# Optimization experiments

Hardware: AMD Instinct MI355X
Metric: run time of the kernel (lower is better)

The kernel has to match this reference:

```python
import jax, jax.numpy as jnp
import numpy as np

N_NODES = 50000
N_EDGES = 800000
N_GRAPHS = 512
D_IN = 128
D_HID = 128
D_OUT = 128
N_CLS = 2


def _deg_inv_sqrt(idx, n):
    deg = jax.ops.segment_sum(jnp.ones(idx.shape[0], jnp.float32), idx, num_segments=n)
    return jnp.where(deg > 0, jax.lax.rsqrt(jnp.maximum(deg, 1.0)), 0.0)


def gcn_conv(x, src, dst, W, b, out_norm, in_norm):
    # DGL GraphConv, norm='both': D_out^{-1/2} on src, sum-aggregate, D_in^{-1/2} on dst, then XW + b
    h = x * out_norm[:, None]                                   # [N, d]
    agg = jax.ops.segment_sum(h[src], dst, num_segments=x.shape[0])  # SpMM: gather + scatter-add
    agg = agg * in_norm[:, None]
    return agg @ W + b


def setup_inputs() -> dict:
    key = jax.random.key(0)
    ks = jax.random.split(key, 8)
    features = jax.random.normal(ks[0], (N_NODES, D_IN), jnp.float32)
    src = jax.random.randint(ks[1], (N_EDGES,), 0, N_NODES, jnp.int32)
    dst = jax.random.randint(ks[2], (N_EDGES,), 0, N_NODES, jnp.int32)
    graph_ids = jnp.sort(jax.random.randint(ks[3], (N_NODES,), 0, N_GRAPHS, jnp.int32))
    W1 = jax.random.normal(ks[4], (D_IN, D_HID), jnp.float32) / np.sqrt(D_IN)
    W2 = jax.random.normal(ks[5], (D_HID, D_OUT), jnp.float32) / np.sqrt(D_HID)
    Wc = jax.random.normal(ks[6], (D_OUT, N_CLS), jnp.float32) / np.sqrt(D_OUT)
    return {
        'features': features, 'src': src, 'dst': dst, 'graph_ids': graph_ids,
        'W1': W1, 'b1': jnp.zeros((D_HID,), jnp.float32),
        'W2': W2, 'b2': jnp.zeros((D_OUT,), jnp.float32),
        'Wc': Wc, 'bc': jnp.zeros((N_CLS,), jnp.float32),
    }


def reference(features, src, dst, graph_ids, W1, b1, W2, b2, Wc, bc):
    n = features.shape[0]
    out_norm = _deg_inv_sqrt(src, n)   # out-degree norm (applied on src side)
    in_norm = _deg_inv_sqrt(dst, n)    # in-degree norm (applied on dst side)
    h = jax.nn.relu(gcn_conv(features, src, dst, W1, b1, out_norm, in_norm))
    h = gcn_conv(h, src, dst, W2, b2, out_norm, in_norm)
    # mean_nodes: segment mean over nodes of each graph
    sums = jax.ops.segment_sum(h, graph_ids, num_segments=N_GRAPHS)          # [G, d]
    cnts = jax.ops.segment_sum(jnp.ones((n,), jnp.float32), graph_ids, num_segments=N_GRAPHS)
    hg = sums / jnp.maximum(cnts, 1.0)[:, None]
    return hg @ Wc + bc
```

## Files before the change

### kernel.cpp

```cpp
#include <hip/hip_runtime.h>
#include <hip/hip_fp16.h>

#define NN 50000
#define NE 800000
#define NG 512
#define DD 128
#define NSB 64
#define SUBN 782
#define SBCAP 14336
#define NB1 512
#define NI4 (NE / 4)
#define CH4 ((NI4 + NB1 - 1) / NB1)

typedef __attribute__((ext_vector_type(8))) _Float16 f16x8;
typedef __attribute__((ext_vector_type(4))) float f32x4;
typedef int v4i __attribute__((ext_vector_type(4)));

__global__ __launch_bounds__(256) void k_f2h(
    const float4* __restrict__ in, const float* __restrict__ out_norm,
    uint2* __restrict__ out, int n4) {
  int i = blockIdx.x * 256 + threadIdx.x;
  if (i >= n4) return;
  float w = out_norm[i >> 5];
  float4 v = in[i];
  __half2 a = __floats2half2_rn(v.x * w, v.y * w);
  __half2 b = __floats2half2_rn(v.z * w, v.w * w);
  uint2 o;
  o.x = *(unsigned int*)&a;
  o.y = *(unsigned int*)&b;
  out[i] = o;
}

__global__ __launch_bounds__(256) void k_prep(
    const float* __restrict__ W1, const float* __restrict__ W2,
    const float* __restrict__ Wc, const float* __restrict__ b2,
    const float* __restrict__ bc,
    _Float16* __restrict__ w1hi, _Float16* __restrict__ w1lo,
    float* __restrict__ w2c, float* __restrict__ zc,
    const int* __restrict__ src, const int* __restrict__ dst,
    int* __restrict__ cur_d, int* __restrict__ cur_s,
    unsigned long long* __restrict__ byDst, unsigned short* __restrict__ bySrc) {
  __shared__ int cntd[NSB], cnts[NSB], based[NSB], bases[NSB];
  int b = blockIdx.x;
  int tid = threadIdx.x;
  if (b < 8) {
    int t = b * 256 + tid;
    int lane = t & 63;
    int grp = t >> 6;
    int kk = grp & 3;
    int nt = grp >> 2;
    int kbase = kk * 32 + ((lane >> 4) << 3);
    int c = nt * 16 + (lane & 15);
#pragma unroll
    for (int j = 0; j < 8; ++j) {
      float v = W1[(kbase + j) * DD + c];
      _Float16 h = (_Float16)v;
      w1hi[t * 8 + j] = h;
      w1lo[t * 8 + j] = (_Float16)(v - (float)h);
    }
  } else if (b == 8) {
    int row = tid >> 1, cc = tid & 1;
    float s = 0.f;
#pragma unroll 8
    for (int c = 0; c < DD; ++c) s += W2[row * DD + c] * Wc[c * 2 + cc];
    w2c[row * 2 + cc] = s;
    if (tid < 2) {
      float bb = 0.f;
      for (int c = 0; c < DD; ++c) bb += b2[c] * Wc[c * 2 + tid];
      zc[tid] = bb + bc[tid];
    }
  } else {
    int i0 = (b - 9) * CH4;
    int i1 = i0 + CH4; if (i1 > NI4) i1 = NI4;
    if (tid < NSB) { cntd[tid] = 0; cnts[tid] = 0; }
    __syncthreads();
    const v4i* s4 = (const v4i*)src;
    const v4i* d4 = (const v4i*)dst;
    for (int i = i0 + tid; i < i1; i += 256) {
      v4i sv = __builtin_nontemporal_load(&s4[i]);
      v4i dv = __builtin_nontemporal_load(&d4[i]);
#pragma unroll
      for (int k = 0; k < 4; ++k) {
        atomicAdd(&cntd[dv[k] / SUBN], 1);
        atomicAdd(&cnts[sv[k] / SUBN], 1);
      }
    }
    __syncthreads();
    if (tid < NSB) {
      based[tid] = atomicAdd(&cur_d[tid], cntd[tid]);
      cntd[tid] = 0;
    } else if (tid < 2 * NSB) {
      int q = tid - NSB;
      bases[q] = atomicAdd(&cur_s[q], cnts[q]);
      cnts[q] = 0;
    }
    __syncthreads();
    for (int i = i0 + tid; i < i1; i += 256) {
      v4i sv = __builtin_nontemporal_load(&s4[i]);
      v4i dv = __builtin_nontemporal_load(&d4[i]);
#pragma unroll
      for (int k = 0; k < 4; ++k) {
        int d = dv[k], s = sv[k];
        int bd = d / SUBN;
        int pd = based[bd] + atomicAdd(&cntd[bd], 1);
        if (pd < SBCAP) byDst[(size_t)bd * SBCAP + pd] = ((unsigned long long)(unsigned)d << 32) | (unsigned)s;
        int bs = s / SUBN;
        int ps = bases[bs] + atomicAdd(&cnts[bs], 1);
        if (ps < SBCAP) bySrc[(size_t)bs * SBCAP + ps] = (unsigned short)(s - bs * SUBN);
      }
    }
  }
}

__global__ __launch_bounds__(1024) void k_csr2(
    const unsigned long long* __restrict__ byDst, const int* __restrict__ cur_d,
    const unsigned short* __restrict__ bySrc, const int* __restrict__ cur_s,
    int* __restrict__ csr, int* __restrict__ row_start, int* __restrict__ deg_in,
    float* __restrict__ in_norm, float* __restrict__ out_norm) {
  __shared__ int hist[SUBN];
  __shared__ int wsum[16];
  int b = blockIdx.x;
  int tid = threadIdx.x;
  if (b < 64) {
    int q = b;
    int nlo = q * SUBN;
    int nhi = nlo + SUBN; if (nhi > NN) nhi = NN;
    int nloc = nhi - nlo;
    for (int i = tid; i < SUBN; i += 1024) hist[i] = 0;
    __syncthreads();
    int m = cur_d[q];
    if (m > SBCAP) m = SBCAP;
    const unsigned long long* bine = byDst + (size_t)q * SBCAP;
    for (int i = tid; i < m; i += 1024) {
      int l = (int)(bine[i] >> 32) - nlo;
      if (l >= 0 && l < nloc) atomicAdd(&hist[l], 1);
    }
    __syncthreads();
    int v = (tid < SUBN) ? hist[tid] : 0;
    int incl = v;
    int lane = tid & 63;
#pragma unroll
    for (int off = 1; off < 64; off <<= 1) {
      int t2 = __shfl_up(incl, off);
      if (lane >= off) incl += t2;
    }
    int wid = tid >> 6;
    if (lane == 63) wsum[wid] = incl;
    __syncthreads();
    if (tid == 0) {
      int run = 0;
      for (int i = 0; i < 16; ++i) { int t = wsum[i]; wsum[i] = run; run += t; }
    }
    __syncthreads();
    int excl = incl - v + wsum[wid];
    if (tid < nloc) {
      deg_in[nlo + tid] = v;
      row_start[nlo + tid] = q * SBCAP + excl;
      in_norm[nlo + tid] = v > 0 ? rsqrtf((float)v) : 0.f;
    }
    __syncthreads();
    if (tid < SUBN) hist[tid] = excl;
    __syncthreads();
    for (int i = tid; i < m; i += 1024) {
      unsigned long long p = bine[i];
      int l = (int)(p >> 32) - nlo;
      if (l >= 0 && l < nloc) {
        int pos = atomicAdd(&hist[l], 1);
        if (pos < SBCAP) csr[(size_t)q * SBCAP + pos] = (int)(unsigned)p;
      }
    }
  } else {
    int q = b - 64;
    int nlo = q * SUBN;
    int nhi = nlo + SUBN; if (nhi > NN) nhi = NN;
    int nloc = nhi - nlo;
    for (int i = tid; i < SUBN; i += 1024) hist[i] = 0;
    __syncthreads();
    int m = cur_s[q];
    if (m > SBCAP) m = SBCAP;
    const unsigned short* bine = bySrc + (size_t)q * SBCAP;
    for (int i = tid; i < m; i += 1024) {
      atomicAdd(&hist[bine[i]], 1);
    }
    __syncthreads();
    for (int i = tid; i < nloc; i += 1024) {
      int od = hist[i];
      out_norm[nlo + i] = od > 0 ? rsqrtf((float)od) : 0.f;
    }
  }
}

__global__ __launch_bounds__(256) void k_agg(
    const __half* __restrict__ x, const int* __restrict__ csr,
    const int* __restrict__ row_start, const int* __restrict__ deg_in,
    __half2* __restrict__ agg) {
  int node = blockIdx.x * 4 + (threadIdx.x >> 6);
  int lane = threadIdx.x & 63;
  if (node >= NN) return;
  int n = deg_in[node];
  const int* bk = csr + row_start[node];
  const __half2* xv = (const __half2*)x;
  float2 a0 = {0.f, 0.f}, a1 = {0.f, 0.f}, a2 = {0.f, 0.f}, a3 = {0.f, 0.f};
  float2 a4 = {0.f, 0.f}, a5 = {0.f, 0.f}, a6 = {0.f, 0.f}, a7 = {0.f, 0.f};
  for (int c0 = 0; c0 < n; c0 += 64) {
    int nn = n - c0; if (nn > 64) nn = 64;
    int sl = (lane < nn) ? bk[c0 + lane] : 0;
    int j = 0;
    for (; j + 8 <= nn; j += 8) {
      int s0 = __shfl(sl, j + 0), s1 = __shfl(sl, j + 1);
      int s2 = __shfl(sl, j + 2), s3 = __shfl(sl, j + 3);
      int s4 = __shfl(sl, j + 4), s5 = __shfl(sl, j + 5);
      int s6 = __shfl(sl, j + 6), s7 = __shfl(sl, j + 7);
      float2 v0 = __half22float2(xv[(size_t)s0 * 64 + lane]);
      float2 v1 = __half22float2(xv[(size_t)s1 * 64 + lane]);
      float2 v2 = __half22float2(xv[(size_t)s2 * 64 + lane]);
      float2 v3 = __half22float2(xv[(size_t)s3 * 64 + lane]);
      float2 v4 = __half22float2(xv[(size_t)s4 * 64 + lane]);
      float2 v5 = __half22float2(xv[(size_t)s5 * 64 + lane]);
      float2 v6 = __half22float2(xv[(size_t)s6 * 64 + lane]);
      float2 v7 = __half22float2(xv[(size_t)s7 * 64 + lane]);
      a0.x += v0.x; a0.y += v0.y;
      a1.x += v1.x; a1.y += v1.y;
      a2.x += v2.x; a2.y += v2.y;
      a3.x += v3.x; a3.y += v3.y;
      a4.x += v4.x; a4.y += v4.y;
      a5.x += v5.x; a5.y += v5.y;
      a6.x += v6.x; a6.y += v6.y;
      a7.x += v7.x; a7.y += v7.y;
    }
    for (; j + 4 <= nn; j += 4) {
      int s0 = __shfl(sl, j + 0), s1 = __shfl(sl, j + 1);
      int s2 = __shfl(sl, j + 2), s3 = __shfl(sl, j + 3);
      float2 v0 = __half22float2(xv[(size_t)s0 * 64 + lane]);
      float2 v1 = __half22float2(xv[(size_t)s1 * 64 + lane]);
      float2 v2 = __half22float2(xv[(size_t)s2 * 64 + lane]);
      float2 v3 = __half22float2(xv[(size_t)s3 * 64 + lane]);
      a0.x += v0.x; a0.y += v0.y;
      a1.x += v1.x; a1.y += v1.y;
      a2.x += v2.x; a2.y += v2.y;
      a3.x += v3.x; a3.y += v3.y;
    }
    for (; j < nn; ++j) {
      int s0 = __shfl(sl, j);
      float2 v0 = __half22float2(xv[(size_t)s0 * 64 + lane]);
      a0.x += v0.x; a0.y += v0.y;
    }
  }
  a0.x += a1.x + a2.x + a3.x + a4.x + a5.x + a6.x + a7.x;
  a0.y += a1.y + a2.y + a3.y + a4.y + a5.y + a6.y + a7.y;
  agg[(size_t)node * 64 + lane] = __floats2half2_rn(a0.x, a0.y);
}

__global__ __launch_bounds__(256, 4) void k_gemm1(
    const __half* __restrict__ A, const float* __restrict__ in_norm,
    const float* __restrict__ out_norm,
    const _Float16* __restrict__ Whi, const _Float16* __restrict__ Wlo,
    const float* __restrict__ bias, const float* __restrict__ W2c,
    float2* __restrict__ p) {
  int tid = threadIdx.x;
  int wid = tid >> 6, lane = tid & 63;
  int row0 = blockIdx.x * 64 + wid * 16;
  int ar = row0 + (lane & 15);
  bool rv = ar < NN;
  f16x8 a_[4];
#pragma unroll
  for (int kk = 0; kk < 4; ++kk) {
    if (rv) {
      a_[kk] = *(const f16x8*)((const _Float16*)A + (size_t)ar * DD + kk * 32 + ((lane >> 4) << 3));
    } else {
      a_[kk] = (f16x8){0, 0, 0, 0, 0, 0, 0, 0};
    }
  }
  f32x4 acc[8];
#pragma unroll
  for (int nt = 0; nt < 8; ++nt) acc[nt] = (f32x4){0.f, 0.f, 0.f, 0.f};
#pragma unroll
  for (int nt = 0; nt < 8; ++nt) {
#pragma unroll
    for (int kk = 0; kk < 4; ++kk) {
      f16x8 bh = *(const f16x8*)&Whi[(((nt * 4 + kk) * 64) + lane) * 8];
      f16x8 bl = *(const f16x8*)&Wlo[(((nt * 4 + kk) * 64) + lane) * 8];
      acc[nt] = __builtin_amdgcn_mfma_f32_16x16x32_f16(a_[kk], bh, acc[nt], 0, 0, 0);
      acc[nt] = __builtin_amdgcn_mfma_f32_16x16x32_f16(a_[kk], bl, acc[nt], 0, 0, 0);
    }
  }
  int r4 = (lane >> 4) * 4;
  int c0 = lane & 15;
  float wc0[8], wc1[8], bv[8];
#pragma unroll
  for (int nt = 0; nt < 8; ++nt) {
    int col = nt * 16 + c0;
    wc0[nt] = W2c[col * 2 + 0];
    wc1[nt] = W2c[col * 2 + 1];
    bv[nt] = bias[col];
  }
#pragma unroll
  for (int reg = 0; reg < 4; ++reg) {
    int row = row0 + r4 + reg;
    float inm = (row < NN) ? in_norm[row] : 0.f;
    float v0 = 0.f, v1 = 0.f;
#pragma unroll
    for (int nt = 0; nt < 8; ++nt) {
      float y = acc[nt][reg] * inm + bv[nt];
      y = fmaxf(y, 0.f);
      v0 += y * wc0[nt];
      v1 += y * wc1[nt];
    }
#pragma unroll
    for (int off = 1; off < 16; off <<= 1) {
      v0 += __shfl_xor(v0, off);
      v1 += __shfl_xor(v1, off);
    }
    if (row < NN && c0 == 0) {
      float onm = out_norm[row];
      p[row] = make_float2(v0 * onm, v1 * onm);
    }
  }
}

__global__ __launch_bounds__(256) void k_agg2(
    const float2* __restrict__ p, const int* __restrict__ csr,
    const int* __restrict__ row_start, const int* __restrict__ deg_in,
    const float* __restrict__ in_norm, float2* __restrict__ z) {
  int i = blockIdx.x * 256 + threadIdx.x;
  if (i >= NN) return;
  int n = deg_in[i];
  const int* bk = csr + row_start[i];
  float2 s0 = {0.f, 0.f}, s1 = {0.f, 0.f}, s2 = {0.f, 0.f}, s3 = {0.f, 0.f};
  int j = 0;
  for (; j + 4 <= n; j += 4) {
    int i0 = bk[j], i1 = bk[j + 1], i2 = bk[j + 2], i3 = bk[j + 3];
    float2 q0 = p[i0], q1 = p[i1], q2 = p[i2], q3 = p[i3];
    s0.x += q0.x; s0.y += q0.y;
    s1.x += q1.x; s1.y += q1.y;
    s2.x += q2.x; s2.y += q2.y;
    s3.x += q3.x; s3.y += q3.y;
  }
  for (; j < n; ++j) {
    float2 q = p[bk[j]];
    s0.x += q.x; s0.y += q.y;
  }
  s0.x += s1.x + s2.x + s3.x;
  s0.y += s1.y + s2.y + s3.y;
  float inm = in_norm[i];
  z[i] = make_float2(s0.x * inm, s0.y * inm);
}

__global__ __launch_bounds__(256) void k_pool2(
    const float* __restrict__ z, const int* __restrict__ gid,
    const float* __restrict__ zc, float* __restrict__ out) {
  int g = blockIdx.x * 4 + (threadIdx.x >> 6);
  int lane = threadIdx.x & 63;
  if (g >= NG) return;
  int lo, hi;
  { int a = 0, b = NN; while (a < b) { int m = (a + b) >> 1; if (gid[m] < g) a = m + 1; else b = m; } lo = a; }
  { int a = lo, b = NN; while (a < b) { int m = (a + b) >> 1; if (gid[m] <= g) a = m + 1; else b = m; } hi = a; }
  float s = 0.f;
  int col = lane & 1;
  for (int i = lo + (lane >> 1); i < hi; i += 32) s += z[i * 2 + col];
#pragma unroll
  for (int off = 32; off >= 2; off >>= 1) s += __shfl_down(s, off);
  if (lane < 2) {
    int n = hi - lo;
    out[g * 2 + lane] = s / (float)(n > 0 ? n : 1) + zc[lane];
  }
}

extern "C" void kernel_launch(void* const* d_in, const int* in_sizes, int n_in,
                              void* d_out, int out_size, void* d_ws, size_t ws_size,
                              hipStream_t stream) {
  const float* features = (const float*)d_in[0];
  const int* src = (const int*)d_in[1];
  const int* dst = (const int*)d_in[2];
  const int* gid = (const int*)d_in[3];
  const float* W1 = (const float*)d_in[4];
  const float* b1 = (const float*)d_in[5];
  const float* W2 = (const float*)d_in[6];
  const float* b2 = (const float*)d_in[7];
  const float* Wc = (const float*)d_in[8];
  const float* bc = (const float*)d_in[9];
  float* out = (float*)d_out;

  char* ws = (char*)d_ws;
  size_t off = 0;
  auto take = [&](size_t bytes) {
    char* p = ws + off;
    off = (off + bytes + 255) & ~(size_t)255;
    return p;
  };
  int* cur_d      = (int*)take(NSB * 4);
  int* cur_s      = (int*)take(NSB * 4);
  int* deg_in     = (int*)take((size_t)NN * 4);
  float* out_nrm  = (float*)take((size_t)NN * 4);
  float* in_nrm   = (float*)take((size_t)NN * 4);
  int* row_start  = (int*)take((size_t)NN * 4);
  float* pbuf     = (float*)take((size_t)NN * 2 * 4);
  float* zbuf     = (float*)take((size_t)NN * 2 * 4);
  float* w2c      = (float*)take((size_t)DD * 2 * 4);
  float* zc       = (float*)take(2 * 4);
  unsigned long long* byDst = (unsigned long long*)take((size_t)NSB * SBCAP * 8);
  unsigned short* bySrc = (unsigned short*)take((size_t)NSB * SBCAP * 2);
  int* csr        = (int*)take((size_t)NSB * SBCAP * 4);
  __half* xh      = (__half*)take((size_t)NN * DD * 2);
  __half* bufA    = (__half*)take((size_t)NN * DD * 2);
  _Float16* w1hi  = (_Float16*)take((size_t)DD * DD * 2);
  _Float16* w1lo  = (_Float16*)take((size_t)DD * DD * 2);

  hipMemsetAsync(cur_d, 0, NSB * 4, stream);
  hipMemsetAsync(cur_s, 0, NSB * 4, stream);

  k_prep<<<NB1 + 9, 256, 0, stream>>>(
      W1, W2, Wc, b2, bc, w1hi, w1lo, w2c, zc,
      src, dst, cur_d, cur_s, byDst, bySrc);

  k_csr2<<<128, 1024, 0, stream>>>(
      byDst, cur_d, bySrc, cur_s, csr, row_start, deg_in, in_nrm, out_nrm);

  k_f2h<<<(NN * 32 + 255) / 256, 256, 0, stream>>>(
      (const float4*)features, out_nrm, (uint2*)xh, NN * 32);

  k_agg<<<(NN + 3) / 4, 256, 0, stream>>>(xh, csr, row_start, deg_in, (__half2*)bufA);
  k_gemm1<<<(NN + 63) / 64, 256, 0, stream>>>(
      bufA, in_nrm, out_nrm, w1hi, w1lo, b1, w2c, (float2*)pbuf);

  k_agg2<<<(NN + 255) / 256, 256, 0, stream>>>(
      (const float2*)pbuf, csr, row_start, deg_in, in_nrm, (float2*)zbuf);

  k_pool2<<<(NG + 3) / 4, 256, 0, stream>>>(zbuf, gid, zc, out);
}
```

Before: 117.8 us.

## Fold fp16 feature conversion into prep kernel and apply out-norm during aggregation

The standalone fp32-to-fp16 conversion kernel is removed and its work is added as extra blocks of the edge-binning prep kernel, so it no longer has to wait for the degree computation. Because out_norm is not available then, the source-side normalisation moves into the aggregation loop as a per-edge weight shuffled across the wave. The two memsets are replaced by one tiny zeroing kernel that assumes cur_d and cur_s are contiguous. The binning histograms are made per-wave to cut LDS atomic contention. In exchange the aggregation does extra multiplies and out_norm gathers, its 4-wide tail loop is dropped, and fp16 rounding now happens before normalisation.

```diff
diff --git a/kernel.cpp b/kernel.cpp
--- a/kernel.cpp
+++ b/kernel.cpp
@@ -11,24 +11,14 @@
 #define NB1 512
 #define NI4 (NE / 4)
 #define CH4 ((NI4 + NB1 - 1) / NB1)
+#define F2HB 6250
 
 typedef __attribute__((ext_vector_type(8))) _Float16 f16x8;
 typedef __attribute__((ext_vector_type(4))) float f32x4;
 typedef int v4i __attribute__((ext_vector_type(4)));
 
-__global__ __launch_bounds__(256) void k_f2h(
-    const float4* __restrict__ in, const float* __restrict__ out_norm,
-    uint2* __restrict__ out, int n4) {
-  int i = blockIdx.x * 256 + threadIdx.x;
-  if (i >= n4) return;
-  float w = out_norm[i >> 5];
-  float4 v = in[i];
-  __half2 a = __floats2half2_rn(v.x * w, v.y * w);
-  __half2 b = __floats2half2_rn(v.z * w, v.w * w);
-  uint2 o;
-  o.x = *(unsigned int*)&a;
-  o.y = *(unsigned int*)&b;
-  out[i] = o;
+__global__ void k_zero(int* __restrict__ p) {
+  p[threadIdx.x] = 0;
 }
 
 __global__ __launch_bounds__(256) void k_prep(
@@ -39,11 +29,22 @@
     float* __restrict__ w2c, float* __restrict__ zc,
     const int* __restrict__ src, const int* __restrict__ dst,
     int* __restrict__ cur_d, int* __restrict__ cur_s,
-    unsigned long long* __restrict__ byDst, unsigned short* __restrict__ bySrc) {
-  __shared__ int cntd[NSB], cnts[NSB], based[NSB], bases[NSB];
+    unsigned long long* __restrict__ byDst, unsigned short* __restrict__ bySrc,
+    const float4* __restrict__ x, uint2* __restrict__ xh) {
+  __shared__ int cntd[4][NSB], cnts[4][NSB], based[NSB], bases[NSB];
+  __shared__ int wbd[4][NSB], wbs[4][NSB];
   int b = blockIdx.x;
   int tid = threadIdx.x;
-  if (b < 8) {
+  if (b >= 521) {
+    int i = (b - 521) * 256 + tid;
+    float4 v = x[i];
+    __half2 a = __floats2half2_rn(v.x, v.y);
+    __half2 c = __floats2half2_rn(v.z, v.w);
+    uint2 o;
+    o.x = *(unsigned int*)&a;
+    o.y = *(unsigned int*)&c;
+    xh[i] = o;
+  } else if (b < 8) {
     int t = b * 256 + tid;
     int lane = t & 63;
     int grp = t >> 6;
@@ -70,9 +71,13 @@
       zc[tid] = bb + bc[tid];
     }
   } else {
+    int w = tid >> 6;
     int i0 = (b - 9) * CH4;
     int i1 = i0 + CH4; if (i1 > NI4) i1 = NI4;
-    if (tid < NSB) { cntd[tid] = 0; cnts[tid] = 0; }
+    if (tid < NSB) {
+#pragma unroll
+      for (int ww = 0; ww < 4; ++ww) { cntd[ww][tid] = 0; cnts[ww][tid] = 0; }
+    }
     __syncthreads();
     const v4i* s4 = (const v4i*)src;
     const v4i* d4 = (const v4i*)dst;
@@ -81,18 +86,26 @@
       v4i dv = __builtin_nontemporal_load(&d4[i]);
 #pragma unroll
       for (int k = 0; k < 4; ++k) {
-        atomicAdd(&cntd[dv[k] / SUBN], 1);
-        atomicAdd(&cnts[sv[k] / SUBN], 1);
+        atomicAdd(&cntd[w][dv[k] / SUBN], 1);
+        atomicAdd(&cnts[w][sv[k] / SUBN], 1);
       }
     }
     __syncthreads();
     if (tid < NSB) {
-      based[tid] = atomicAdd(&cur_d[tid], cntd[tid]);
-      cntd[tid] = 0;
+      int run = 0;
+#pragma unroll
+      for (int ww = 0; ww < 4; ++ww) { wbd[ww][tid] = run; run += cntd[ww][tid]; }
+      based[tid] = atomicAdd(&cur_d[tid], run);
+#pragma unroll
+      for (int ww = 0; ww < 4; ++ww) cntd[ww][tid] = 0;
     } else if (tid < 2 * NSB) {
       int q = tid - NSB;
-      bases[q] = atomicAdd(&cur_s[q], cnts[q]);
-      cnts[q] = 0;
+      int run = 0;
+#pragma unroll
+      for (int ww = 0; ww < 4; ++ww) { wbs[ww][q] = run; run += cnts[ww][q]; }
+      bases[q] = atomicAdd(&cur_s[q], run);
+#pragma unroll
+      for (int ww = 0; ww < 4; ++ww) cnts[ww][q] = 0;
     }
     __syncthreads();
     for (int i = i0 + tid; i < i1; i += 256) {
@@ -102,10 +115,10 @@
       for (int k = 0; k < 4; ++k) {
         int d = dv[k], s = sv[k];
         int bd = d / SUBN;
-        int pd = based[bd] + atomicAdd(&cntd[bd], 1);
+        int pd = based[bd] + wbd[w][bd] + atomicAdd(&cntd[w][bd], 1);
         if (pd < SBCAP) byDst[(size_t)bd * SBCAP + pd] = ((unsigned long long)(unsigned)d << 32) | (unsigned)s;
         int bs = s / SUBN;
-        int ps = bases[bs] + atomicAdd(&cnts[bs], 1);
+        int ps = bases[bs] + wbs[w][bs] + atomicAdd(&cnts[w][bs], 1);
         if (ps < SBCAP) bySrc[(size_t)bs * SBCAP + ps] = (unsigned short)(s - bs * SUBN);
       }
     }
@@ -193,7 +206,7 @@
 __global__ __launch_bounds__(256) void k_agg(
     const __half* __restrict__ x, const int* __restrict__ csr,
     const int* __restrict__ row_start, const int* __restrict__ deg_in,
-    __half2* __restrict__ agg) {
+    const float* __restrict__ out_norm, __half2* __restrict__ agg) {
   int node = blockIdx.x * 4 + (threadIdx.x >> 6);
   int lane = threadIdx.x & 63;
   if (node >= NN) return;
@@ -204,13 +217,18 @@
   float2 a4 = {0.f, 0.f}, a5 = {0.f, 0.f}, a6 = {0.f, 0.f}, a7 = {0.f, 0.f};
   for (int c0 = 0; c0 < n; c0 += 64) {
     int nn = n - c0; if (nn > 64) nn = 64;
-    int sl = (lane < nn) ? bk[c0 + lane] : 0;
+    int sl = 0; float wl = 0.f;
+    if (lane < nn) { sl = bk[c0 + lane]; wl = out_norm[sl]; }
     int j = 0;
     for (; j + 8 <= nn; j += 8) {
       int s0 = __shfl(sl, j + 0), s1 = __shfl(sl, j + 1);
       int s2 = __shfl(sl, j + 2), s3 = __shfl(sl, j + 3);
       int s4 = __shfl(sl, j + 4), s5 = __shfl(sl, j + 5);
       int s6 = __shfl(sl, j + 6), s7 = __shfl(sl, j + 7);
+      float w0 = __shfl(wl, j + 0), w1 = __shfl(wl, j + 1);
+      float w2 = __shfl(wl, j + 2), w3 = __shfl(wl, j + 3);
+      float w4 = __shfl(wl, j + 4), w5 = __shfl(wl, j + 5);
+      float w6 = __shfl(wl, j + 6), w7 = __shfl(wl, j + 7);
       float2 v0 = __half22float2(xv[(size_t)s0 * 64 + lane]);
       float2 v1 = __half22float2(xv[(size_t)s1 * 64 + lane]);
       float2 v2 = __half22float2(xv[(size_t)s2 * 64 + lane]);
@@ -219,31 +237,20 @@
       float2 v5 = __half22float2(xv[(size_t)s5 * 64 + lane]);
       float2 v6 = __half22float2(xv[(size_t)s6 * 64 + lane]);
       float2 v7 = __half22float2(xv[(size_t)s7 * 64 + lane]);
-      a0.x += v0.x; a0.y += v0.y;
-      a1.x += v1.x; a1.y += v1.y;
-      a2.x += v2.x; a2.y += v2.y;
-      a3.x += v3.x; a3.y += v3.y;
-      a4.x += v4.x; a4.y += v4.y;
-      a5.x += v5.x; a5.y += v5.y;
-      a6.x += v6.x; a6.y += v6.y;
-      a7.x += v7.x; a7.y += v7.y;
-    }
-    for (; j + 4 <= nn; j += 4) {
-      int s0 = __shfl(sl, j + 0), s1 = __shfl(sl, j + 1);
-      int s2 = __shfl(sl, j + 2), s3 = __shfl(sl, j + 3);
-      float2 v0 = __half22float2(xv[(size_t)s0 * 64 + lane]);
-      float2 v1 = __half22float2(xv[(size_t)s1 * 64 + lane]);
-      float2 v2 = __half22float2(xv[(size_t)s2 * 64 + lane]);
-      float2 v3 = __half22float2(xv[(size_t)s3 * 64 + lane]);
-      a0.x += v0.x; a0.y += v0.y;
-      a1.x += v1.x; a1.y += v1.y;
-      a2.x += v2.x; a2.y += v2.y;
-      a3.x += v3.x; a3.y += v3.y;
+      a0.x += v0.x * w0; a0.y += v0.y * w0;
+      a1.x += v1.x * w1; a1.y += v1.y * w1;
+      a2.x += v2.x * w2; a2.y += v2.y * w2;
+      a3.x += v3.x * w3; a3.y += v3.y * w3;
+      a4.x += v4.x * w4; a4.y += v4.y * w4;
+      a5.x += v5.x * w5; a5.y += v5.y * w5;
+      a6.x += v6.x * w6; a6.y += v6.y * w6;
+      a7.x += v7.x * w7; a7.y += v7.y * w7;
     }
     for (; j < nn; ++j) {
       int s0 = __shfl(sl, j);
+      float w0 = __shfl(wl, j);
       float2 v0 = __half22float2(xv[(size_t)s0 * 64 + lane]);
-      a0.x += v0.x; a0.y += v0.y;
+      a0.x += v0.x * w0; a0.y += v0.y * w0;
     }
   }
   a0.x += a1.x + a2.x + a3.x + a4.x + a5.x + a6.x + a7.x;
@@ -406,20 +413,18 @@
   _Float16* w1hi  = (_Float16*)take((size_t)DD * DD * 2);
   _Float16* w1lo  = (_Float16*)take((size_t)DD * DD * 2);
 
-  hipMemsetAsync(cur_d, 0, NSB * 4, stream);
-  hipMemsetAsync(cur_s, 0, NSB * 4, stream);
-
-  k_prep<<<NB1 + 9, 256, 0, stream>>>(
+  k_zero<<<1, 128, 0, stream>>>(cur_d);
+
+  k_prep<<<521 + F2HB, 256, 0, stream>>>(
       W1, W2, Wc, b2, bc, w1hi, w1lo, w2c, zc,
-      src, dst, cur_d, cur_s, byDst, bySrc);
+      src, dst, cur_d, cur_s, byDst, bySrc,
+      (const float4*)features, (uint2*)xh);
 
   k_csr2<<<128, 1024, 0, stream>>>(
       byDst, cur_d, bySrc, cur_s, csr, row_start, deg_in, in_nrm, out_nrm);
 
-  k_f2h<<<(NN * 32 + 255) / 256, 256, 0, stream>>>(
-      (const float4*)features, out_nrm, (uint2*)xh, NN * 32);
-
-  k_agg<<<(NN + 3) / 4, 256, 0, stream>>>(xh, csr, row_start, deg_in, (__half2*)bufA);
+  k_agg<<<(NN + 3) / 4, 256, 0, stream>>>(
+      xh, csr, row_start, deg_in, out_nrm, (__half2*)bufA);
   k_gemm1<<<(NN + 63) / 64, 256, 0, stream>>>(
       bufA, in_nrm, out_nrm, w1hi, w1lo, b1, w2c, (float2*)pbuf);
 
```

Result: no change. 116.3 us (-1.3%).
